# Kernel optimization log

Measured on AMD Instinct MI355X. Metric: run time of the kernel, lower is better.

## Reference

```python
import jax, jax.numpy as jnp
import numpy as np

H, B = 128, 8          # hidden_channels, num_bilinear
NR, NS = 6, 7          # num_radial, num_spherical
E, T = 100000, 262144  # num_edges (rows of x), num_triplets


def _glorot(key, shape):
    fan = shape[-2] + shape[-1]
    return jax.random.normal(key, shape, jnp.float32) * jnp.sqrt(2.0 / fan)


def setup_inputs() -> dict:
    key = jax.random.key(0)
    ks = jax.random.split(key, 16)
    return {
        "x": jax.random.normal(ks[0], (E, H), jnp.float32),
        "radial_basis": jax.random.normal(ks[1], (E, NR), jnp.float32),
        "spherical_basis": jax.random.normal(ks[2], (T, NS * NR), jnp.float32),
        "edge_index_from": jax.random.randint(ks[3], (T,), 0, E, jnp.int32),
        "edge_index_to": jax.random.randint(ks[4], (T,), 0, E, jnp.int32),
        "w_rbf": _glorot(ks[5], (NR, H)),
        "w_sbf": _glorot(ks[6], (NS * NR, B)),
        "w_from": _glorot(ks[7], (H, H)),
        "b_from": jnp.zeros((H,), jnp.float32),
        "w_to": _glorot(ks[8], (H, H)),
        "b_to": jnp.zeros((H,), jnp.float32),
        "W": jax.random.normal(ks[9], (H, B, H), jnp.float32) * (2.0 / H),
        "rb_w": _glorot(ks[10], (1, 2, H, H)),
        "rb_b": jnp.zeros((1, 2, H), jnp.float32),
        "lin_w": _glorot(ks[11], (H, H)),
        "lin_b": jnp.zeros((H,), jnp.float32),
        "ra_w": _glorot(ks[12], (2, 2, H, H)),
        "ra_b": jnp.zeros((2, 2, H), jnp.float32),
    }


def _residual(h, w, b):
    # DimeNet ResidualLayer: h + act(lin2(act(lin1(h))))
    act = jax.nn.silu
    return h + act(act(h @ w[0] + b[0]) @ w[1] + b[1])


def reference(x, radial_basis, spherical_basis, edge_index_from, edge_index_to,
              w_rbf, w_sbf, w_from, b_from, w_to, b_to, W,
              rb_w, rb_b, lin_w, lin_b, ra_w, ra_b):
    act = jax.nn.silu
    rbf = radial_basis @ w_rbf                      # [E, H]
    sbf = spherical_basis @ w_sbf                   # [T, B]
    x_kj = act(x @ w_from + b_from) * rbf           # [E, H]
    gathered = x_kj[edge_index_from]                # [T, H] irregular gather
    # bilinear: out[w,i] = sum_{j,l} sbf[w,j] * gathered[w,l] * W[i,j,l]
    msg = jnp.einsum('wj,wl,ijl->wi', sbf, gathered, W, optimize=True)  # [T, H]
    agg = jax.ops.segment_sum(msg, edge_index_to, num_segments=x.shape[0])  # [E, H]
    x_ji = act(x @ w_to + b_to)
    h = x_ji + agg
    for i in range(rb_w.shape[0]):
        h = _residual(h, rb_w[i], rb_b[i])
    h = act(h @ lin_w + lin_b) + x
    for i in range(ra_w.shape[0]):
        h = _residual(h, ra_w[i], ra_b[i])
    return h
```

## Files before the change

kernel.cpp:

```cpp
#include <hip/hip_runtime.h>
#include <cstdint>


#define H 128
#define NB 8
#define NR 6
#define SBC 42
#define LDA 136
#define LDF 132
#define WFRAG 16384

using f16x8 = __attribute__((ext_vector_type(8))) _Float16;
using f32x4 = __attribute__((ext_vector_type(4))) float;

__device__ __forceinline__ float silu_f(float v){
  return v / (1.f + __expf(-v));
}
__device__ __forceinline__ f16x8 pack8(float4 a, float4 b){
  f16x8 h;
  h[0]=(_Float16)a.x; h[1]=(_Float16)a.y; h[2]=(_Float16)a.z; h[3]=(_Float16)a.w;
  h[4]=(_Float16)b.x; h[5]=(_Float16)b.y; h[6]=(_Float16)b.z; h[7]=(_Float16)b.w;
  return h;
}
__device__ __forceinline__ void lds_dma16(const void* g, void* l){
  __builtin_amdgcn_global_load_lds(
      (const __attribute__((address_space(1))) unsigned int*)g,
      (__attribute__((address_space(3))) unsigned int*)l, 16, 0, 0);
}
__device__ __forceinline__ void atomic_pk_add_f16(_Float16* addr, float lo, float hi){
  union { _Float16 h[2]; unsigned u; } d;
  d.h[0] = (_Float16)lo; d.h[1] = (_Float16)hi;
  asm volatile("global_atomic_pk_add_f16 %0, %1, off"
               :: "v"(addr), "v"(d.u) : "memory");
}

__global__ void prep_kernel(const float* __restrict__ w_from,
                            const float* __restrict__ w_to,
                            const float* __restrict__ rb_w,
                            const float* __restrict__ lin_w,
                            const float* __restrict__ ra_w,
                            const float* __restrict__ Wb,
                            _Float16* __restrict__ wf,
                            _Float16* __restrict__ Wf)
{
  int idx = blockIdx.x*256 + threadIdx.x;
  if (blockIdx.x < 72){
    int m = idx >> 11, c = idx & 2047;
    int nt = c >> 8, kk = (c>>6)&3, l = c&63, q = l>>4, l15 = l&15;
    const float* src;
    switch(m){
      case 0: src = w_from;       break;
      case 1: src = w_to;         break;
      case 2: src = rb_w;         break;
      case 3: src = rb_w + 16384; break;
      case 4: src = lin_w;        break;
      case 5: src = ra_w;         break;
      case 6: src = ra_w + 16384; break;
      case 7: src = ra_w + 32768; break;
      default: src = ra_w + 49152; break;
    }
    const float* p = src + (size_t)(kk*32 + q*8)*H + nt*16 + l15;
    f16x8 o;
    #pragma unroll
    for (int j=0;j<8;j++) o[j] = (_Float16)p[(size_t)j*H];
    *reinterpret_cast<f16x8*>(wf + (size_t)m*WFRAG + c*8) = o;
  } else {
    int t = idx - 72*256;
    int j = t >> 11, c = t & 2047;
    int nt = c >> 8, kk = (c>>6)&3, l = c&63, q = l>>4, l15 = l&15;
    const float4* p = reinterpret_cast<const float4*>(
        Wb + ((size_t)(nt*16+l15)*NB + j)*H + kk*32 + q*8);
    *reinterpret_cast<f16x8*>(Wf + (size_t)j*WFRAG + c*8) = pack8(p[0], p[1]);
  }
}

__global__ __launch_bounds__(256,2) void edge_kernel(
    const float* __restrict__ x,
    const float* __restrict__ radial,
    const float* __restrict__ w_rbf,
    const _Float16* __restrict__ wf,
    const float* __restrict__ b_from,
    const float* __restrict__ b_to,
    _Float16* __restrict__ x_kj, _Float16* __restrict__ agg, int E)
{
  __shared__ alignas(16) _Float16 sA[64*LDA];
  __shared__ alignas(16) _Float16 sB[WFRAG];
  __shared__ alignas(16) _Float16 sO[64*LDA];
  __shared__ float sRad[64*8];
  __shared__ float sWr[128*8];
  __shared__ float sBf[128];
  __shared__ float sBt[128];
  int tid = threadIdx.x;
  int e0 = blockIdx.x*64;
  int wave = tid>>6, lane = tid&63, l15 = lane&15, q = lane>>4;

  const uint4* wfu = reinterpret_cast<const uint4*>(wf);
  const uint4* wtu = reinterpret_cast<const uint4*>(wf + WFRAG);
  uint4* sBu = reinterpret_cast<uint4*>(sB);
  uint4 wr[8];
  #pragma unroll
  for (int i=0;i<8;i++) wr[i] = wfu[i*256 + tid];

  {
    int row = tid>>2, cs = (tid&3)*32;
    bool ok = (e0+row) < E;
    const float4* src = reinterpret_cast<const float4*>(x + (size_t)(e0+row)*H + cs);
    #pragma unroll
    for (int i=0;i<4;i++){
      float4 u0{0,0,0,0}, u1{0,0,0,0};
      if (ok){ u0 = src[2*i]; u1 = src[2*i+1]; }
      *reinterpret_cast<f16x8*>(&sA[row*LDA + cs + i*8]) = pack8(u0,u1);
    }
  }
  for (int i=tid; i<64*NR; i+=256){
    int r=i/NR, c=i%NR;
    sRad[r*8+c] = (e0+r < E) ? radial[(size_t)(e0+r)*NR + c] : 0.f;
  }
  for (int i=tid; i<NR*H; i+=256){
    int c=i>>7, n=i&127;
    sWr[n*8+c] = w_rbf[i];
  }
  if (tid < H){ sBf[tid] = b_from[tid]; sBt[tid] = b_to[tid]; }
  #pragma unroll
  for (int i=0;i<8;i++) sBu[i*256 + tid] = wr[i];
  #pragma unroll
  for (int i=0;i<8;i++) wr[i] = wtu[i*256 + tid];
  __syncthreads();

  f32x4 acc[8];
  auto gemm = [&](){
    #pragma unroll
    for (int nt=0;nt<8;nt++) acc[nt] = f32x4{0.f,0.f,0.f,0.f};
    int ar = (wave*16 + l15)*LDA;
    #pragma unroll
    for (int kk=0;kk<4;kk++){
      f16x8 a = *reinterpret_cast<const f16x8*>(&sA[ar + kk*32 + q*8]);
      #pragma unroll
      for (int nt=0;nt<8;nt++){
        f16x8 b = *reinterpret_cast<const f16x8*>(&sB[((nt*4+kk)*64 + lane)*8]);
        acc[nt] = __builtin_amdgcn_mfma_f32_16x16x32_f16(a, b, acc[nt], 0,0,0);
      }
    }
  };

  gemm();
  __syncthreads();
  #pragma unroll
  for (int nt=0;nt<8;nt++)
    #pragma unroll
    for (int r=0;r<4;r++){
      int rl = wave*16 + q*4 + r, col = nt*16 + l15;
      float v = silu_f(acc[nt][r] + sBf[col]);
      float rb = 0.f;
      #pragma unroll
      for (int c=0;c<NR;c++) rb += sRad[rl*8+c]*sWr[col*8+c];
      sO[rl*LDA+col] = (_Float16)(v*rb);
    }
  #pragma unroll
  for (int i=0;i<8;i++) sBu[i*256 + tid] = wr[i];
  __syncthreads();
  {
    int row=tid>>2, cs=(tid&3)*32;
    if (e0+row < E)
      #pragma unroll
      for (int i=0;i<4;i++)
        *reinterpret_cast<f16x8*>(x_kj + (size_t)(e0+row)*H + cs + i*8) =
          *reinterpret_cast<const f16x8*>(&sO[row*LDA + cs + i*8]);
  }
  gemm();
  __syncthreads();
  #pragma unroll
  for (int nt=0;nt<8;nt++)
    #pragma unroll
    for (int r=0;r<4;r++){
      int rl = wave*16 + q*4 + r, col = nt*16 + l15;
      sO[rl*LDA+col] = (_Float16)silu_f(acc[nt][r] + sBt[col]);
    }
  __syncthreads();
  {
    int row=tid>>2, cs=(tid&3)*32;
    if (e0+row < E)
      #pragma unroll
      for (int i=0;i<4;i++)
        *reinterpret_cast<f16x8*>(agg + (size_t)(e0+row)*H + cs + i*8) =
          *reinterpret_cast<const f16x8*>(&sO[row*LDA + cs + i*8]);
  }
}

__global__ __launch_bounds__(256,3) void bilinear_kernel(
    const _Float16* __restrict__ x_kj,
    const float* __restrict__ sph,
    const float* __restrict__ w_sbf,
    const _Float16* __restrict__ Wf,
    const int* __restrict__ e_from, const int* __restrict__ e_to,
    _Float16* __restrict__ agg)
{
  __shared__ alignas(16) _Float16 wch[WFRAG];
  __shared__ float ssb[128*NB];
  __shared__ float sw[SBC*NB];
  __shared__ int sdst[128];
  int tid = threadIdx.x;
  long long t0 = (long long)blockIdx.x * 128;
  int wave = tid>>6, lane = tid&63, l15 = lane&15, q = lane>>4;
  int m0 = wave*32;

  int ef0 = e_from[t0 + m0 + l15];
  int ef1 = e_from[t0 + m0 + 16 + l15];
  f16x8 aR0[4], aR1[4];
  #pragma unroll
  for (int kk=0;kk<4;kk++){
    aR0[kk] = *reinterpret_cast<const f16x8*>(x_kj + (size_t)ef0*H + kk*32 + q*8);
    aR1[kk] = *reinterpret_cast<const f16x8*>(x_kj + (size_t)ef1*H + kk*32 + q*8);
  }

  {
    float4* scr = reinterpret_cast<float4*>(wch);
    const float4* g = reinterpret_cast<const float4*>(sph + t0*SBC);
    for (int i=tid; i<128*SBC/4; i+=256) scr[i] = g[i];
  }
  for (int i=tid; i<SBC*NB; i+=256) sw[i] = w_sbf[i];
  if (tid < 128) sdst[tid] = e_to[t0 + tid];
  __syncthreads();
  {
    int row = tid>>1, half = tid&1;
    const float* srow = reinterpret_cast<const float*>(wch) + row*SBC;
    float a4[4] = {0.f,0.f,0.f,0.f};
    for (int c=0;c<SBC;c++){
      float v = srow[c];
      #pragma unroll
      for (int cc=0;cc<4;cc++) a4[cc] += v * sw[c*NB + half*4 + cc];
    }
    #pragma unroll
    for (int cc=0;cc<4;cc++) ssb[row*NB + half*4 + cc] = a4[cc];
  }

  f32x4 acc[2][8];
  #pragma unroll
  for (int mt=0;mt<2;mt++)
    #pragma unroll
    for (int nt=0;nt<8;nt++) acc[mt][nt] = f32x4{0.f,0.f,0.f,0.f};

  for (int jj=0;jj<NB;jj++){
    __syncthreads();
    {
      const _Float16* gs = Wf + (size_t)jj*WFRAG + (size_t)(wave*64 + lane)*8;
      _Float16* ls = wch + (size_t)(wave*64)*8;
      #pragma unroll
      for (int u=0;u<8;u++)
        lds_dma16(gs + (size_t)u*2048, ls + (size_t)u*2048);
    }
    __syncthreads();
    _Float16 s0 = (_Float16)ssb[(m0+l15)*NB + jj];
    _Float16 s1 = (_Float16)ssb[(m0+16+l15)*NB + jj];
    #pragma unroll
    for (int kk=0;kk<4;kk++){
      f16x8 a0 = aR0[kk] * s0;
      f16x8 a1 = aR1[kk] * s1;
      #pragma unroll
      for (int nt=0;nt<8;nt++){
        f16x8 b = *reinterpret_cast<const f16x8*>(&wch[((nt*4+kk)*64 + lane)*8]);
        acc[0][nt] = __builtin_amdgcn_mfma_f32_16x16x32_f16(a0, b, acc[0][nt], 0,0,0);
        acc[1][nt] = __builtin_amdgcn_mfma_f32_16x16x32_f16(a1, b, acc[1][nt], 0,0,0);
      }
    }
  }

  int odd = l15 & 1;
  #pragma unroll
  for (int mt=0;mt<2;mt++)
    #pragma unroll
    for (int ntp=0;ntp<4;ntp++)
      #pragma unroll
      for (int r=0;r<4;r++){
        float a = acc[mt][2*ntp  ][r];
        float b = acc[mt][2*ntp+1][r];
        float ax = __shfl_xor(a, 1);
        float bx = __shfl_xor(b, 1);
        int rl  = m0 + mt*16 + q*4 + r;
        int col = 32*ntp + (odd ? 15 + l15 : l15);
        atomic_pk_add_f16(agg + (size_t)sdst[rl]*H + col,
                          odd ? bx : a, odd ? b : ax);
      }
}

__global__ __launch_bounds__(256,3) void post_kernel(
    const float* __restrict__ x, const _Float16* __restrict__ agg,
    const _Float16* __restrict__ wf,
    const float* __restrict__ rb_b, const float* __restrict__ lin_b,
    const float* __restrict__ ra_b,
    float* __restrict__ out, int E)
{
  __shared__ alignas(16) _Float16 smem[64*LDA + WFRAG];
  __shared__ float sBias[128];
  _Float16* sIn = smem;
  _Float16* sW  = smem + 64*LDA;
  uint4* sWu = reinterpret_cast<uint4*>(sW);
  int tid = threadIdx.x, e0 = blockIdx.x*64;
  int wave = tid>>6, lane = tid&63, l15 = lane&15, q = lane>>4;

  const float* bptr[7] = {rb_b, rb_b+128, lin_b, ra_b, ra_b+128, ra_b+256, ra_b+384};

  uint4 wr[8];
  {
    const uint4* wp = reinterpret_cast<const uint4*>(wf + 2*WFRAG);
    #pragma unroll
    for (int u=0;u<8;u++) wr[u] = wp[u*256 + tid];
  }

  {
    int row=tid>>2, cs=(tid&3)*32;
    bool ok = (e0+row) < E;
    f16x8 z;
    #pragma unroll
    for (int j=0;j<8;j++) z[j] = (_Float16)0.f;
    #pragma unroll
    for (int i=0;i<4;i++){
      f16x8 v = z;
      if (ok) v = *reinterpret_cast<const f16x8*>(agg + (size_t)(e0+row)*H + cs + i*8);
      *reinterpret_cast<f16x8*>(&sIn[row*LDA + cs + i*8]) = v;
    }
  }
  __syncthreads();
  float h[8][4];
  #pragma unroll
  for (int nt=0;nt<8;nt++)
    #pragma unroll
    for (int r=0;r<4;r++)
      h[nt][r] = (float)sIn[(wave*16+q*4+r)*LDA + nt*16 + l15];

  f32x4 acc[8];
  #pragma unroll
  for (int s=0;s<7;s++){
    #pragma unroll
    for (int u=0;u<8;u++) sWu[u*256 + tid] = wr[u];
    if (tid < H) sBias[tid] = bptr[s][tid];
    if (s < 6){
      const uint4* wp = reinterpret_cast<const uint4*>(wf + (size_t)(3+s)*WFRAG);
      #pragma unroll
      for (int u=0;u<8;u++) wr[u] = wp[u*256 + tid];
    }
    __syncthreads();
    #pragma unroll
    for (int nt=0;nt<8;nt++) acc[nt] = f32x4{0.f,0.f,0.f,0.f};
    int ar = (wave*16 + l15)*LDA;
    #pragma unroll
    for (int kk=0;kk<4;kk++){
      f16x8 a = *reinterpret_cast<const f16x8*>(&sIn[ar + kk*32 + q*8]);
      #pragma unroll
      for (int nt=0;nt<8;nt++){
        f16x8 b = *reinterpret_cast<const f16x8*>(&sW[((nt*4+kk)*64 + lane)*8]);
        acc[nt] = __builtin_amdgcn_mfma_f32_16x16x32_f16(a, b, acc[nt], 0,0,0);
      }
    }
    __syncthreads();
    #pragma unroll
    for (int nt=0;nt<8;nt++)
      #pragma unroll
      for (int r=0;r<4;r++){
        int rl = wave*16 + q*4 + r, col = nt*16 + l15;
        float v = silu_f(acc[nt][r] + sBias[col]);
        if (s==0 || s==3 || s==5){
          sIn[rl*LDA+col] = (_Float16)v;
        } else if (s==1 || s==4){
          h[nt][r] += v;
          sIn[rl*LDA+col] = (_Float16)h[nt][r];
        } else if (s==2){
          bool ok = (e0+rl) < E;
          float xv = ok ? x[(size_t)(e0+rl)*H + col] : 0.f;
          h[nt][r] = v + xv;
          sIn[rl*LDA+col] = (_Float16)h[nt][r];
        } else {
          h[nt][r] += v;
          reinterpret_cast<float*>(smem)[rl*LDF+col] = h[nt][r];
        }
      }
  }
  __syncthreads();
  {
    const float* scr = reinterpret_cast<const float*>(smem);
    int row=tid>>2, cs=(tid&3)*32;
    if (e0+row < E)
      #pragma unroll
      for (int i=0;i<8;i++)
        *reinterpret_cast<float4*>(out + (size_t)(e0+row)*H + cs + i*4) =
          *reinterpret_cast<const float4*>(&scr[row*LDF + cs + i*4]);
  }
}

extern "C" void kernel_launch(void* const* d_in, const int* in_sizes, int n_in,
                              void* d_out, int out_size, void* d_ws, size_t ws_size,
                              hipStream_t stream)
{
  const float* x      = (const float*)d_in[0];
  const float* radial = (const float*)d_in[1];
  const float* sph    = (const float*)d_in[2];
  const int* e_from   = (const int*)d_in[3];
  const int* e_to     = (const int*)d_in[4];
  const float* w_rbf  = (const float*)d_in[5];
  const float* w_sbf  = (const float*)d_in[6];
  const float* w_from = (const float*)d_in[7];
  const float* b_from = (const float*)d_in[8];
  const float* w_to   = (const float*)d_in[9];
  const float* b_to   = (const float*)d_in[10];
  const float* Wb     = (const float*)d_in[11];
  const float* rb_w   = (const float*)d_in[12];
  const float* rb_b   = (const float*)d_in[13];
  const float* lin_w  = (const float*)d_in[14];
  const float* lin_b  = (const float*)d_in[15];
  const float* ra_w   = (const float*)d_in[16];
  const float* ra_b   = (const float*)d_in[17];

  int E = in_sizes[0] / H;
  int T = in_sizes[3];

  char* ws = (char*)d_ws;
  _Float16* aggh = (_Float16*)ws;
  _Float16* wf   = (_Float16*)(ws + (size_t)E*H*2);
  _Float16* Wf   = wf + 9*WFRAG;
  _Float16* x_kj = (_Float16*)d_out;

  prep_kernel<<<136, 256, 0, stream>>>(w_from, w_to, rb_w, lin_w, ra_w, Wb, wf, Wf);
  edge_kernel<<<(E+63)/64, 256, 0, stream>>>(x, radial, w_rbf, wf, b_from, b_to,
                                             x_kj, aggh, E);
  bilinear_kernel<<<T/128, 256, 0, stream>>>(x_kj, sph, w_sbf, Wf, e_from, e_to, aggh);
  post_kernel<<<(E+63)/64, 256, 0, stream>>>(x, aggh, wf, rb_b, lin_b, ra_b,
                                             (float*)d_out, E);
}
```

Baseline: 460.2 us.

## Read MFMA weight fragments directly from global memory instead of LDS staging

In both edge_kernel and post_kernel, weight fragments are now loaded straight from global or L2 into registers per k-step, rather than staged into shared memory. This frees LDS so occupancy bounds rise (edge 2→3, post 3→4 blocks). The bias buffer is double-buffered so the per-stage weight-staging barrier is no longer needed. The trade-off is that every wave re-reads the weights from cache, adding global-load latency inside the GEMM loop.

```diff
diff --git a/kernel.cpp b/kernel.cpp
--- a/kernel.cpp
+++ b/kernel.cpp
@@ -74,7 +74,7 @@
   }
 }
 
-__global__ __launch_bounds__(256,2) void edge_kernel(
+__global__ __launch_bounds__(256,3) void edge_kernel(
     const float* __restrict__ x,
     const float* __restrict__ radial,
     const float* __restrict__ w_rbf,
@@ -84,7 +84,6 @@
     _Float16* __restrict__ x_kj, _Float16* __restrict__ agg, int E)
 {
   __shared__ alignas(16) _Float16 sA[64*LDA];
-  __shared__ alignas(16) _Float16 sB[WFRAG];
   __shared__ alignas(16) _Float16 sO[64*LDA];
   __shared__ float sRad[64*8];
   __shared__ float sWr[128*8];
@@ -94,13 +93,6 @@
   int e0 = blockIdx.x*64;
   int wave = tid>>6, lane = tid&63, l15 = lane&15, q = lane>>4;
 
-  const uint4* wfu = reinterpret_cast<const uint4*>(wf);
-  const uint4* wtu = reinterpret_cast<const uint4*>(wf + WFRAG);
-  uint4* sBu = reinterpret_cast<uint4*>(sB);
-  uint4 wr[8];
-  #pragma unroll
-  for (int i=0;i<8;i++) wr[i] = wfu[i*256 + tid];
-
   {
     int row = tid>>2, cs = (tid&3)*32;
     bool ok = (e0+row) < E;
@@ -121,30 +113,28 @@
     sWr[n*8+c] = w_rbf[i];
   }
   if (tid < H){ sBf[tid] = b_from[tid]; sBt[tid] = b_to[tid]; }
-  #pragma unroll
-  for (int i=0;i<8;i++) sBu[i*256 + tid] = wr[i];
-  #pragma unroll
-  for (int i=0;i<8;i++) wr[i] = wtu[i*256 + tid];
   __syncthreads();
 
   f32x4 acc[8];
-  auto gemm = [&](){
+  auto gemm = [&](const _Float16* wsl){
     #pragma unroll
     for (int nt=0;nt<8;nt++) acc[nt] = f32x4{0.f,0.f,0.f,0.f};
     int ar = (wave*16 + l15)*LDA;
+    const _Float16* wl = wsl + (size_t)lane*8;
     #pragma unroll
     for (int kk=0;kk<4;kk++){
+      f16x8 bfr[8];
+      #pragma unroll
+      for (int nt=0;nt<8;nt++)
+        bfr[nt] = *reinterpret_cast<const f16x8*>(wl + (size_t)(nt*4+kk)*512);
       f16x8 a = *reinterpret_cast<const f16x8*>(&sA[ar + kk*32 + q*8]);
       #pragma unroll
-      for (int nt=0;nt<8;nt++){
-        f16x8 b = *reinterpret_cast<const f16x8*>(&sB[((nt*4+kk)*64 + lane)*8]);
-        acc[nt] = __builtin_amdgcn_mfma_f32_16x16x32_f16(a, b, acc[nt], 0,0,0);
-      }
+      for (int nt=0;nt<8;nt++)
+        acc[nt] = __builtin_amdgcn_mfma_f32_16x16x32_f16(a, bfr[nt], acc[nt], 0,0,0);
     }
   };
 
-  gemm();
-  __syncthreads();
+  gemm(wf);
   #pragma unroll
   for (int nt=0;nt<8;nt++)
     #pragma unroll
@@ -156,8 +146,6 @@
       for (int c=0;c<NR;c++) rb += sRad[rl*8+c]*sWr[col*8+c];
       sO[rl*LDA+col] = (_Float16)(v*rb);
     }
-  #pragma unroll
-  for (int i=0;i<8;i++) sBu[i*256 + tid] = wr[i];
   __syncthreads();
   {
     int row=tid>>2, cs=(tid&3)*32;
@@ -167,7 +155,7 @@
         *reinterpret_cast<f16x8*>(x_kj + (size_t)(e0+row)*H + cs + i*8) =
           *reinterpret_cast<const f16x8*>(&sO[row*LDA + cs + i*8]);
   }
-  gemm();
+  gemm(wf + WFRAG);
   __syncthreads();
   #pragma unroll
   for (int nt=0;nt<8;nt++)
@@ -283,29 +271,20 @@
       }
 }
 
-__global__ __launch_bounds__(256,3) void post_kernel(
+__global__ __launch_bounds__(256,4) void post_kernel(
     const float* __restrict__ x, const _Float16* __restrict__ agg,
     const _Float16* __restrict__ wf,
     const float* __restrict__ rb_b, const float* __restrict__ lin_b,
     const float* __restrict__ ra_b,
     float* __restrict__ out, int E)
 {
-  __shared__ alignas(16) _Float16 smem[64*LDA + WFRAG];
-  __shared__ float sBias[128];
+  __shared__ alignas(16) _Float16 smem[64*LDF*2];
+  __shared__ float sBias[2][128];
   _Float16* sIn = smem;
-  _Float16* sW  = smem + 64*LDA;
-  uint4* sWu = reinterpret_cast<uint4*>(sW);
   int tid = threadIdx.x, e0 = blockIdx.x*64;
   int wave = tid>>6, lane = tid&63, l15 = lane&15, q = lane>>4;
 
   const float* bptr[7] = {rb_b, rb_b+128, lin_b, ra_b, ra_b+128, ra_b+256, ra_b+384};
-
-  uint4 wr[8];
-  {
-    const uint4* wp = reinterpret_cast<const uint4*>(wf + 2*WFRAG);
-    #pragma unroll
-    for (int u=0;u<8;u++) wr[u] = wp[u*256 + tid];
-  }
 
   {
     int row=tid>>2, cs=(tid&3)*32;
@@ -331,26 +310,22 @@
   f32x4 acc[8];
   #pragma unroll
   for (int s=0;s<7;s++){
-    #pragma unroll
-    for (int u=0;u<8;u++) sWu[u*256 + tid] = wr[u];
-    if (tid < H) sBias[tid] = bptr[s][tid];
-    if (s < 6){
-      const uint4* wp = reinterpret_cast<const uint4*>(wf + (size_t)(3+s)*WFRAG);
-      #pragma unroll
-      for (int u=0;u<8;u++) wr[u] = wp[u*256 + tid];
-    }
+    if (tid < H) sBias[s&1][tid] = bptr[s][tid];
     __syncthreads();
     #pragma unroll
     for (int nt=0;nt<8;nt++) acc[nt] = f32x4{0.f,0.f,0.f,0.f};
     int ar = (wave*16 + l15)*LDA;
+    const _Float16* wl = wf + (size_t)(s+2)*WFRAG + (size_t)lane*8;
     #pragma unroll
     for (int kk=0;kk<4;kk++){
+      f16x8 bfr[8];
+      #pragma unroll
+      for (int nt=0;nt<8;nt++)
+        bfr[nt] = *reinterpret_cast<const f16x8*>(wl + (size_t)(nt*4+kk)*512);
       f16x8 a = *reinterpret_cast<const f16x8*>(&sIn[ar + kk*32 + q*8]);
       #pragma unroll
-      for (int nt=0;nt<8;nt++){
-        f16x8 b = *reinterpret_cast<const f16x8*>(&sW[((nt*4+kk)*64 + lane)*8]);
-        acc[nt] = __builtin_amdgcn_mfma_f32_16x16x32_f16(a, b, acc[nt], 0,0,0);
-      }
+      for (int nt=0;nt<8;nt++)
+        acc[nt] = __builtin_amdgcn_mfma_f32_16x16x32_f16(a, bfr[nt], acc[nt], 0,0,0);
     }
     __syncthreads();
     #pragma unroll
@@ -358,7 +333,7 @@
       #pragma unroll
       for (int r=0;r<4;r++){
         int rl = wave*16 + q*4 + r, col = nt*16 + l15;
-        float v = silu_f(acc[nt][r] + sBias[col]);
+        float v = silu_f(acc[nt][r] + sBias[s&1][col]);
         if (s==0 || s==3 || s==5){
           sIn[rl*LDA+col] = (_Float16)v;
         } else if (s==1 || s==4){
```

Result: faster. 414.6 us (-9.9%).
